# Performance work log

Hardware: AMD Instinct MI355X
Metric: run time of the kernel (lower is better)

## Reference

```python
import jax, jax.numpy as jnp
import numpy as np

NUM_HEADS = 8
IN_CH = 256  # C per branch; x has 2*C channels
DHW = (16, 16, 16)


def _proj(w, b, feat):
    # 1x1x1 Conv3d == per-voxel linear over channels. w: [Co, Ci], feat: [B, Ci, D, H, W]
    return jnp.einsum('oc,bcdhw->bodhw', w, feat) + b[None, :, None, None, None]


def _rope(n, dim):
    # matches rotary_embedding: returns [dim, n]
    inv_freq = 1.0 / (10000.0 ** (jnp.arange(0, dim, 2, dtype=jnp.float32) / dim))
    pos = jnp.linspace(-1.0, 1.0, n)
    sinusoid = pos[:, None] * inv_freq[None, :]          # [n, dim//2]
    emb = jnp.concatenate([jnp.sin(sinusoid), jnp.cos(sinusoid)], axis=-1)  # [n, dim]
    return emb.T                                          # [dim, n]


def setup_inputs() -> dict:
    key = jax.random.key(0)
    ks = jax.random.split(key, 5)
    D, H, W = DHW
    C = IN_CH
    s = 0.05
    return {
        'x': jax.random.normal(ks[0], (1, 2 * C, D, H, W), dtype=jnp.float32),
        'wq': jax.random.normal(ks[1], (C, C), dtype=jnp.float32) * s,
        'bq': jnp.zeros((C,), jnp.float32),
        'wk': jax.random.normal(ks[2], (C, C), dtype=jnp.float32) * s,
        'bk': jnp.zeros((C,), jnp.float32),
        'wv': jax.random.normal(ks[3], (C, C), dtype=jnp.float32) * s,
        'bv': jnp.zeros((C,), jnp.float32),
        'wo': jax.random.normal(ks[4], (2 * C, C), dtype=jnp.float32) * s,
        'bo': jnp.zeros((2 * C,), jnp.float32),
    }


def reference(x, wq, bq, wk, bk, wv, bv, wo, bo):
    qf, kvf = jnp.split(x, 2, axis=1)          # each [B, C, D, H, W]
    B, C, D, H, W = qf.shape
    hd = C // NUM_HEADS
    N = D * H * W
    q = _proj(wq, bq, qf).reshape(B, NUM_HEADS, hd, N)
    k = _proj(wk, bk, kvf).reshape(B, NUM_HEADS, hd, N)
    v = _proj(wv, bv, kvf).reshape(B, NUM_HEADS, hd, N)
    pe = _rope(N, hd)                           # [hd, N]
    q = q * pe[None, None]
    k = k * pe[None, None]
    attn = jnp.einsum('bhcn,bhcm->bhnm', q, k)  # note: no 1/sqrt(d) scaling, as in source
    attn = jax.nn.softmax(attn, axis=-1)
    out = jnp.einsum('bhnm,bhcm->bhcn', attn, v).reshape(B, C, D, H, W)
    return _proj(wo, bo, out + qf)              # [B, 2C, D, H, W]
```

## Files before the change

kernel.cpp:

```cpp
#include <hip/hip_runtime.h>
#include <hip/hip_bf16.h>

#define CIN 256
#define NV 4096
#define NHEAD 8
#define HD 32
#define NSPLIT 2
#define KSPAN (NV / NSPLIT)
#define LOG2E 1.44269504088896340736f
#define LOG2_10K_16 0.8304820237218405f

typedef __attribute__((ext_vector_type(8))) short short8;
typedef __attribute__((ext_vector_type(4))) float f32x4;

static __device__ __forceinline__ unsigned short f2bf(float f) {
    union { float f; unsigned u; } v; v.f = f;
    unsigned r = v.u + 0x7fffu + ((v.u >> 16) & 1u);
    return (unsigned short)(r >> 16);
}
static __device__ __forceinline__ unsigned pk_bf2(float x0, float x1) {
    return __builtin_amdgcn_perm(__float_as_uint(x1), __float_as_uint(x0),
                                 0x07060302u);
}
static __device__ __forceinline__ float bflo(unsigned u) {
    return __uint_as_float(u << 16);
}
static __device__ __forceinline__ float bfhi(unsigned u) {
    return __uint_as_float(u & 0xffff0000u);
}

__global__ __launch_bounds__(256) void conv_w(
    const float* __restrict__ wq, const float* __restrict__ wk,
    const float* __restrict__ wv, const float* __restrict__ wo,
    unsigned short* __restrict__ Wb)
{
    int i = (blockIdx.x * 256 + threadIdx.x) * 4;
    if (i >= 327680) return;
    const float* src;
    int off = i;
    if (i < 65536) { src = wq; }
    else if (i < 131072) { src = wk; off = i - 65536; }
    else if (i < 196608) { src = wv; off = i - 131072; }
    else { src = wo; off = i - 196608; }
    float4 v = *(const float4*)&src[off];
    unsigned short pk[4] = {f2bf(v.x), f2bf(v.y), f2bf(v.z), f2bf(v.w)};
    *(uint2*)&Wb[i] = *(uint2*)pk;
}

__global__ __launch_bounds__(512) void qkv_fused(
    const float* __restrict__ x, const unsigned short* __restrict__ Wb,
    const float* __restrict__ bq, const float* __restrict__ bk,
    const float* __restrict__ bv,
    unsigned short* __restrict__ Qbf, unsigned short* __restrict__ Kbf,
    unsigned short* __restrict__ Vbf)
{
    const int which = blockIdx.z;
    const unsigned short* Wp = Wb + (size_t)which * 65536;
    const float* Bp = (which == 0) ? bq : (which == 1) ? bk : bv;
    const int cbase = (which == 0) ? 0 : CIN;

    const int n0 = blockIdx.x * 64;
    const int m0 = blockIdx.y * 128;
    const int t = threadIdx.x;

    __shared__ __align__(16) unsigned short Sbuf[128 * 136];

    {
        const int n = t & 63, cg = t >> 6;
#pragma unroll 4
        for (int cc = 0; cc < 32; cc += 2) {
            const int c = cg * 32 + cc;
            size_t off = (size_t)(cbase + c) * NV + n0 + n;
            *(unsigned*)&Sbuf[n * 264 + c] = pk_bf2(x[off], x[off + NV]);
        }
    }
    __syncthreads();

    const int w = t >> 6;
    const int lane = t & 63;
    const int ln = lane & 15;
    const int quad = lane >> 4;
    const int M = m0 + w * 16 + ln;

    f32x4 acc[4] = {};
    const unsigned short* Wrow = &Wp[(size_t)M * 256 + quad * 8];
    for (int k0 = 0; k0 < 256; k0 += 32) {
        short8 a = *(const short8*)&Wrow[k0];
        short8 b[4];
#pragma unroll
        for (int nt = 0; nt < 4; ++nt)
            b[nt] = *(const short8*)&Sbuf[(nt * 16 + ln) * 264 + k0 + quad * 8];
        if (which == 2) {
#pragma unroll
            for (int nt = 0; nt < 4; ++nt)
                acc[nt] = __builtin_amdgcn_mfma_f32_16x16x32_bf16(
                    b[nt], a, acc[nt], 0, 0, 0);
        } else {
#pragma unroll
            for (int nt = 0; nt < 4; ++nt)
                acc[nt] = __builtin_amdgcn_mfma_f32_16x16x32_bf16(
                    a, b[nt], acc[nt], 0, 0, 0);
        }
    }
    __syncthreads();

    if (which == 2) {
        const int cl = w * 16 + ln;
        const float bias = Bp[m0 + cl];
#pragma unroll
        for (int nt = 0; nt < 4; ++nt) {
            unsigned short pk4[4];
#pragma unroll
            for (int r = 0; r < 4; ++r) pk4[r] = f2bf(acc[nt][r] + bias);
            *(uint2*)&Sbuf[cl * 136 + nt * 16 + quad * 4] = *(uint2*)pk4;
        }
        __syncthreads();
#pragma unroll
        for (int j = 0; j < 2; ++j) {
            int gid = j * 512 + t;
            int n8 = (gid & 7) * 8, cl2 = gid >> 3;
            uint4 v = *(const uint4*)&Sbuf[cl2 * 136 + n8];
            *(uint4*)&Vbf[(size_t)(m0 + cl2) * NV + n0 + n8] = v;
        }
    } else {
        const int mb = m0 + w * 16 + quad * 4;
        const int cb = mb & 31;
        const float qscale = (which == 0) ? LOG2E : 1.0f;
        float bias[4], invf[4];
#pragma unroll
        for (int r = 0; r < 4; ++r) {
            bias[r] = Bp[mb + r];
            invf[r] = __builtin_amdgcn_exp2f(
                -(float)((cb + r) & 15) * LOG2_10K_16);
        }
        const bool use_sin = (cb < 16);
        const int ml = w * 16 + quad * 4;
#pragma unroll
        for (int nt = 0; nt < 4; ++nt) {
            const int n = n0 + nt * 16 + ln;
            const float pos = (float)n * (2.0f / 4095.0f) - 1.0f;
#pragma unroll
            for (int r = 0; r < 4; ++r) {
                float ang = pos * invf[r];
                float f = (use_sin ? __sinf(ang) : __cosf(ang)) * qscale;
                Sbuf[(nt * 16 + ln) * 264 + ml + r] =
                    f2bf((acc[nt][r] + bias[r]) * f);
            }
        }
        __syncthreads();
        unsigned short* dst = (which == 0) ? Qbf : Kbf;
        const int h0 = m0 >> 5;
#pragma unroll
        for (int j = 0; j < 2; ++j) {
            int gid = j * 512 + t;
            int c8 = (gid & 3) * 8;
            int n = (gid >> 2) & 63;
            int hh = gid >> 8;
            uint4 v = *(const uint4*)&Sbuf[n * 264 + hh * 32 + c8];
            *(uint4*)&dst[((size_t)(h0 + hh) * NV + n0 + n) * HD + c8] = v;
        }
    }
}

__global__ __launch_bounds__(256, 4) void attn_mfma(
    const unsigned short* __restrict__ Qbf,
    const unsigned short* __restrict__ Kbf,
    const unsigned short* __restrict__ Vbf,
    unsigned short* __restrict__ Opartb, float* __restrict__ Lpart)
{
    const int h = blockIdx.y;
    const int q0 = blockIdx.x * 64;
    const int z = blockIdx.z;
    const int kbase = z * KSPAN;
    const int t = threadIdx.x;
    const int w = t >> 6;
    const int lane = t & 63;
    const int ln = lane & 15;
    const int quad = lane >> 4;

    __shared__ __align__(16) unsigned short Vs[2][2048];

    const short8 qa = *(const short8*)
        &Qbf[((size_t)h * NV + q0 + w * 16 + ln) * HD + quad * 8];

    const unsigned short* Kh = Kbf + (size_t)h * NV * HD;
    const unsigned short* Vh = Vbf + (size_t)h * HD * NV;

    const int c_st = (w << 3) + (lane >> 3);
    const int gr_st = (lane & 7) ^ (c_st & 7);
    const unsigned short* gsrc = Vh + (size_t)c_st * NV + gr_st * 8;
    unsigned short* lds0 = &Vs[0][(size_t)(w * 64 + lane) * 8];
    unsigned short* lds1 = &Vs[1][(size_t)(w * 64 + lane) * 8];

    f32x4 oacc[2] = {};
    f32x4 lacc = {};
    const short vone = (short)0x3F80;
    const short8 vones = {vone, vone, vone, vone, vone, vone, vone, vone};

    __builtin_amdgcn_global_load_lds(
        (const __attribute__((address_space(1))) unsigned int*)(gsrc + kbase),
        (__attribute__((address_space(3))) unsigned int*)lds0, 16, 0, 0);
    short8 kf[4];
#pragma unroll
    for (int ct = 0; ct < 4; ++ct)
        kf[ct] = *(const short8*)
            &Kh[(size_t)(kbase + ct * 16 + ln) * HD + quad * 8];
    __syncthreads();

    for (int i = 0; i < KSPAN / 64; ++i) {
        const int kb = kbase + i * 64;
        const int buf = i & 1;

        if (i + 1 < KSPAN / 64) {
            __builtin_amdgcn_global_load_lds(
                (const __attribute__((address_space(1))) unsigned int*)(gsrc + kb + 64),
                (__attribute__((address_space(3))) unsigned int*)(buf ? lds0 : lds1),
                16, 0, 0);
        }
        const int kbn = kbase + (((i + 1) & (KSPAN / 64 - 1)) * 64);
        short8 kfn[4];
#pragma unroll
        for (int ct = 0; ct < 4; ++ct)
            kfn[ct] = *(const short8*)
                &Kh[(size_t)(kbn + ct * 16 + ln) * HD + quad * 8];

        f32x4 s[4];
#pragma unroll
        for (int ct = 0; ct < 4; ++ct) {
            f32x4 z4 = {0.f, 0.f, 0.f, 0.f};
            s[ct] = __builtin_amdgcn_mfma_f32_16x16x32_bf16(kf[ct], qa, z4,
                                                            0, 0, 0);
        }

        float p[4][4];
#pragma unroll
        for (int ct = 0; ct < 4; ++ct)
#pragma unroll
            for (int r = 0; r < 4; ++r)
                p[ct][r] = __builtin_amdgcn_exp2f(s[ct][r]);

#pragma unroll
        for (int h2 = 0; h2 < 2; ++h2) {
            short8 pa;
            unsigned* pau = (unsigned*)&pa;
            pau[0] = pk_bf2(p[2 * h2][0], p[2 * h2][1]);
            pau[1] = pk_bf2(p[2 * h2][2], p[2 * h2][3]);
            pau[2] = pk_bf2(p[2 * h2 + 1][0], p[2 * h2 + 1][1]);
            pau[3] = pk_bf2(p[2 * h2 + 1][2], p[2 * h2 + 1][3]);
            lacc = __builtin_amdgcn_mfma_f32_16x16x32_bf16(pa, vones, lacc,
                                                           0, 0, 0);
#pragma unroll
            for (int ctile = 0; ctile < 2; ++ctile) {
                const int cA = ctile * 16 + ln;
                short8 vb;
                unsigned* vbu = (unsigned*)&vb;
#pragma unroll
                for (int g = 0; g < 2; ++g) {
                    const int gr = h2 * 4 + g * 2 + (quad >> 1);
                    const int sg = gr ^ (ln & 7);
                    uint2 vv = *(const uint2*)
                        &Vs[buf][cA * 64 + sg * 8 + (quad & 1) * 4];
                    vbu[g * 2 + 0] = vv.x;
                    vbu[g * 2 + 1] = vv.y;
                }
                oacc[ctile] = __builtin_amdgcn_mfma_f32_16x16x32_bf16(
                    pa, vb, oacc[ctile], 0, 0, 0);
            }
        }

#pragma unroll
        for (int ct = 0; ct < 4; ++ct) kf[ct] = kfn[ct];
        __syncthreads();
    }

    unsigned short* Oz = Opartb + (size_t)z * CIN * NV;
    float* Lz = Lpart + (size_t)z * NHEAD * NV;
    if (ln == 0) {
#pragma unroll
        for (int r = 0; r < 4; ++r)
            Lz[(size_t)h * NV + q0 + w * 16 + quad * 4 + r] = lacc[r];
    }
#pragma unroll
    for (int ctile = 0; ctile < 2; ++ctile) {
        uint2 st;
        st.x = pk_bf2(oacc[ctile][0], oacc[ctile][1]);
        st.y = pk_bf2(oacc[ctile][2], oacc[ctile][3]);
        *(uint2*)&Oz[(size_t)(h * HD + ctile * 16 + ln) * NV + q0 + w * 16 +
                     quad * 4] = st;
    }
}

__global__ __launch_bounds__(512) void out_fused(
    const float* __restrict__ x,
    const unsigned short* __restrict__ O0b,
    const unsigned short* __restrict__ O1b,
    const float* __restrict__ Lpart,
    const unsigned short* __restrict__ Wob, const float* __restrict__ bo,
    float* __restrict__ out)
{
    const int n0 = blockIdx.x * 64;
    const int m0 = blockIdx.y * 128;
    const int t = threadIdx.x;

    __shared__ __align__(16) unsigned short Ys[64 * 264];

    const float* L0 = Lpart;
    const float* L1 = Lpart + (size_t)NHEAD * NV;

    {
        const int n2 = (t & 31) * 2;
        const int grp = t >> 5;
        const int h = grp >> 1;
        const size_t lo = (size_t)h * NV + n0 + n2;
        const float rl0 = __builtin_amdgcn_rcpf(L0[lo] + L1[lo]);
        const float rl1 = __builtin_amdgcn_rcpf(L0[lo + 1] + L1[lo + 1]);
#pragma unroll 4
        for (int i = 0; i < 16; ++i) {
            const int c = grp * 16 + i;
            size_t off = (size_t)c * NV + n0 + n2;
            unsigned o0 = *(const unsigned*)&O0b[off];
            unsigned o1 = *(const unsigned*)&O1b[off];
            float2 x2 = *(const float2*)&x[off];
            float y0 = (bflo(o0) + bflo(o1)) * rl0 + x2.x;
            float y1 = (bfhi(o0) + bfhi(o1)) * rl1 + x2.y;
            Ys[n2 * 264 + c] = f2bf(y0);
            Ys[(n2 + 1) * 264 + c] = f2bf(y1);
        }
    }
    __syncthreads();

    const int w = t >> 6;
    const int lane = t & 63;
    const int ln = lane & 15;
    const int quad = lane >> 4;
    const int M = m0 + w * 16 + ln;

    const unsigned short* Wrow = &Wob[(size_t)M * 256 + quad * 8];
    f32x4 acc[4] = {};
    for (int k0 = 0; k0 < 256; k0 += 32) {
        short8 a = *(const short8*)&Wrow[k0];
        short8 b[4];
#pragma unroll
        for (int nt = 0; nt < 4; ++nt)
            b[nt] = *(const short8*)&Ys[(nt * 16 + ln) * 264 + k0 + quad * 8];
#pragma unroll
        for (int nt = 0; nt < 4; ++nt)
            acc[nt] = __builtin_amdgcn_mfma_f32_16x16x32_bf16(
                a, b[nt], acc[nt], 0, 0, 0);
    }

    const int mb = m0 + w * 16 + quad * 4;
    float bias[4];
#pragma unroll
    for (int r = 0; r < 4; ++r) bias[r] = bo[mb + r];
#pragma unroll
    for (int nt = 0; nt < 4; ++nt)
#pragma unroll
        for (int r = 0; r < 4; ++r)
            out[(size_t)(mb + r) * NV + n0 + nt * 16 + ln] =
                acc[nt][r] + bias[r];
}

extern "C" void kernel_launch(void* const* d_in, const int* in_sizes, int n_in,
                              void* d_out, int out_size, void* d_ws,
                              size_t ws_size, hipStream_t stream)
{
    const float* x  = (const float*)d_in[0];
    const float* wq = (const float*)d_in[1];
    const float* bq = (const float*)d_in[2];
    const float* wk = (const float*)d_in[3];
    const float* bk = (const float*)d_in[4];
    const float* wv = (const float*)d_in[5];
    const float* bv = (const float*)d_in[6];
    const float* wo = (const float*)d_in[7];
    const float* bo = (const float*)d_in[8];
    float* out = (float*)d_out;

    unsigned short* Wb  = (unsigned short*)d_ws;
    unsigned short* Qbf = Wb + 327680;
    unsigned short* Kbf = Qbf + (size_t)CIN * NV;
    unsigned short* Vbf = Kbf + (size_t)CIN * NV;
    float* Lpart = (float*)(Vbf + (size_t)CIN * NV);
    unsigned short* Opartb =
        (unsigned short*)(Lpart + 2 * (size_t)NHEAD * NV);

    conv_w<<<dim3(320), 256, 0, stream>>>(wq, wk, wv, wo, Wb);
    qkv_fused<<<dim3(64, 2, 3), 512, 0, stream>>>(
        x, Wb, bq, bk, bv, Qbf, Kbf, Vbf);
    attn_mfma<<<dim3(NV / 64, NHEAD, NSPLIT), 256, 0, stream>>>(
        Qbf, Kbf, Vbf, Opartb, Lpart);
    out_fused<<<dim3(64, 4), 512, 0, stream>>>(
        x, Opartb, Opartb + (size_t)CIN * NV, Lpart, Wb + 196608, bo, out);
}
```

Measured before the change: 129.0 us.

## Split attention keys four ways, stage K in LDS, shrink projection tiles

Raises the key-split factor for attention from 2 to 4, so twice as many blocks run and the GPU is filled more evenly. The partial outputs and normalisers are reduced generically in the output kernel. K tiles now go into swizzled LDS through async global_load_lds, double-buffered alongside V, replacing per-lane register prefetch. The V fragment read becomes a single 16-byte LDS load. The QKV and output projection kernels halve their voxel tile to 32 to double the grid. The costs are more partial-sum traffic and reduction work in the epilogue, and less reuse per projection block.

```diff
diff --git a/kernel.cpp b/kernel.cpp
--- a/kernel.cpp
+++ b/kernel.cpp
@@ -5,7 +5,7 @@
 #define NV 4096
 #define NHEAD 8
 #define HD 32
-#define NSPLIT 2
+#define NSPLIT 4
 #define KSPAN (NV / NSPLIT)
 #define LOG2E 1.44269504088896340736f
 #define LOG2_10K_16 0.8304820237218405f
@@ -59,17 +59,17 @@
     const float* Bp = (which == 0) ? bq : (which == 1) ? bk : bv;
     const int cbase = (which == 0) ? 0 : CIN;
 
-    const int n0 = blockIdx.x * 64;
+    const int n0 = blockIdx.x * 32;
     const int m0 = blockIdx.y * 128;
     const int t = threadIdx.x;
 
-    __shared__ __align__(16) unsigned short Sbuf[128 * 136];
+    __shared__ __align__(16) unsigned short Sbuf[32 * 264];
 
     {
-        const int n = t & 63, cg = t >> 6;
+        const int n = t & 31, cg = t >> 5;
 #pragma unroll 4
-        for (int cc = 0; cc < 32; cc += 2) {
-            const int c = cg * 32 + cc;
+        for (int cc = 0; cc < 16; cc += 2) {
+            const int c = cg * 16 + cc;
             size_t off = (size_t)(cbase + c) * NV + n0 + n;
             *(unsigned*)&Sbuf[n * 264 + c] = pk_bf2(x[off], x[off + NV]);
         }
@@ -82,22 +82,22 @@
     const int quad = lane >> 4;
     const int M = m0 + w * 16 + ln;
 
-    f32x4 acc[4] = {};
+    f32x4 acc[2] = {};
     const unsigned short* Wrow = &Wp[(size_t)M * 256 + quad * 8];
     for (int k0 = 0; k0 < 256; k0 += 32) {
         short8 a = *(const short8*)&Wrow[k0];
-        short8 b[4];
-#pragma unroll
-        for (int nt = 0; nt < 4; ++nt)
+        short8 b[2];
+#pragma unroll
+        for (int nt = 0; nt < 2; ++nt)
             b[nt] = *(const short8*)&Sbuf[(nt * 16 + ln) * 264 + k0 + quad * 8];
         if (which == 2) {
 #pragma unroll
-            for (int nt = 0; nt < 4; ++nt)
+            for (int nt = 0; nt < 2; ++nt)
                 acc[nt] = __builtin_amdgcn_mfma_f32_16x16x32_bf16(
                     b[nt], a, acc[nt], 0, 0, 0);
         } else {
 #pragma unroll
-            for (int nt = 0; nt < 4; ++nt)
+            for (int nt = 0; nt < 2; ++nt)
                 acc[nt] = __builtin_amdgcn_mfma_f32_16x16x32_bf16(
                     a, b[nt], acc[nt], 0, 0, 0);
         }
@@ -108,19 +108,20 @@
         const int cl = w * 16 + ln;
         const float bias = Bp[m0 + cl];
 #pragma unroll
-        for (int nt = 0; nt < 4; ++nt) {
+        for (int nt = 0; nt < 2; ++nt) {
             unsigned short pk4[4];
 #pragma unroll
             for (int r = 0; r < 4; ++r) pk4[r] = f2bf(acc[nt][r] + bias);
-            *(uint2*)&Sbuf[cl * 136 + nt * 16 + quad * 4] = *(uint2*)pk4;
+            *(uint2*)&Sbuf[cl * 40 + nt * 16 + quad * 4] = *(uint2*)pk4;
         }
         __syncthreads();
-#pragma unroll
-        for (int j = 0; j < 2; ++j) {
-            int gid = j * 512 + t;
-            int n8 = (gid & 7) * 8, cl2 = gid >> 3;
-            uint4 v = *(const uint4*)&Sbuf[cl2 * 136 + n8];
-            *(uint4*)&Vbf[(size_t)(m0 + cl2) * NV + n0 + n8] = v;
+        {
+            const int cl2 = t >> 2, q = t & 3;
+            uint2 lo = *(const uint2*)&Sbuf[cl2 * 40 + q * 4];
+            uint2 hi = *(const uint2*)&Sbuf[cl2 * 40 + 16 + q * 4];
+            uint4 v;
+            v.x = lo.x; v.y = lo.y; v.z = hi.x; v.w = hi.y;
+            *(uint4*)&Vbf[(size_t)(m0 + cl2) * NV + n0 + q * 8] = v;
         }
     } else {
         const int mb = m0 + w * 16 + quad * 4;
@@ -136,7 +137,7 @@
         const bool use_sin = (cb < 16);
         const int ml = w * 16 + quad * 4;
 #pragma unroll
-        for (int nt = 0; nt < 4; ++nt) {
+        for (int nt = 0; nt < 2; ++nt) {
             const int n = n0 + nt * 16 + ln;
             const float pos = (float)n * (2.0f / 4095.0f) - 1.0f;
 #pragma unroll
@@ -150,14 +151,12 @@
         __syncthreads();
         unsigned short* dst = (which == 0) ? Qbf : Kbf;
         const int h0 = m0 >> 5;
-#pragma unroll
-        for (int j = 0; j < 2; ++j) {
-            int gid = j * 512 + t;
-            int c8 = (gid & 3) * 8;
-            int n = (gid >> 2) & 63;
-            int hh = gid >> 8;
-            uint4 v = *(const uint4*)&Sbuf[n * 264 + hh * 32 + c8];
-            *(uint4*)&dst[((size_t)(h0 + hh) * NV + n0 + n) * HD + c8] = v;
+        {
+            const int hh = t >> 7;
+            const int n = (t >> 2) & 31;
+            const int cw = t & 3;
+            uint4 v = *(const uint4*)&Sbuf[n * 264 + hh * 32 + cw * 8];
+            *(uint4*)&dst[((size_t)(h0 + hh) * NV + n0 + n) * HD + cw * 8] = v;
         }
     }
 }
@@ -178,6 +177,7 @@
     const int ln = lane & 15;
     const int quad = lane >> 4;
 
+    __shared__ __align__(16) unsigned short Ks[2][2048];
     __shared__ __align__(16) unsigned short Vs[2][2048];
 
     const short8 qa = *(const short8*)
@@ -186,11 +186,11 @@
     const unsigned short* Kh = Kbf + (size_t)h * NV * HD;
     const unsigned short* Vh = Vbf + (size_t)h * HD * NV;
 
-    const int c_st = (w << 3) + (lane >> 3);
-    const int gr_st = (lane & 7) ^ (c_st & 7);
-    const unsigned short* gsrc = Vh + (size_t)c_st * NV + gr_st * 8;
-    unsigned short* lds0 = &Vs[0][(size_t)(w * 64 + lane) * 8];
-    unsigned short* lds1 = &Vs[1][(size_t)(w * 64 + lane) * 8];
+    const int cv = t >> 3;
+    const unsigned short* gsrcV = Vh + (size_t)cv * NV + ((t & 7) ^ (cv & 7)) * 8;
+    const int kv = t >> 2;
+    const unsigned short* gsrcK =
+        Kh + (size_t)kv * HD + ((t & 3) ^ (kv & 3)) * 8;
 
     f32x4 oacc[2] = {};
     f32x4 lacc = {};
@@ -198,37 +198,39 @@
     const short8 vones = {vone, vone, vone, vone, vone, vone, vone, vone};
 
     __builtin_amdgcn_global_load_lds(
-        (const __attribute__((address_space(1))) unsigned int*)(gsrc + kbase),
-        (__attribute__((address_space(3))) unsigned int*)lds0, 16, 0, 0);
-    short8 kf[4];
-#pragma unroll
-    for (int ct = 0; ct < 4; ++ct)
-        kf[ct] = *(const short8*)
-            &Kh[(size_t)(kbase + ct * 16 + ln) * HD + quad * 8];
+        (const __attribute__((address_space(1))) unsigned int*)(gsrcK +
+            (size_t)kbase * HD),
+        (__attribute__((address_space(3))) unsigned int*)&Ks[0][t * 8], 16, 0, 0);
+    __builtin_amdgcn_global_load_lds(
+        (const __attribute__((address_space(1))) unsigned int*)(gsrcV + kbase),
+        (__attribute__((address_space(3))) unsigned int*)&Vs[0][t * 8], 16, 0, 0);
     __syncthreads();
 
+    const int sgk = (quad ^ (ln & 3)) * 8;
     for (int i = 0; i < KSPAN / 64; ++i) {
         const int kb = kbase + i * 64;
         const int buf = i & 1;
 
         if (i + 1 < KSPAN / 64) {
             __builtin_amdgcn_global_load_lds(
-                (const __attribute__((address_space(1))) unsigned int*)(gsrc + kb + 64),
-                (__attribute__((address_space(3))) unsigned int*)(buf ? lds0 : lds1),
+                (const __attribute__((address_space(1))) unsigned int*)(gsrcK +
+                    (size_t)(kb + 64) * HD),
+                (__attribute__((address_space(3))) unsigned int*)&Ks[buf ^ 1][t * 8],
                 16, 0, 0);
-        }
-        const int kbn = kbase + (((i + 1) & (KSPAN / 64 - 1)) * 64);
-        short8 kfn[4];
-#pragma unroll
-        for (int ct = 0; ct < 4; ++ct)
-            kfn[ct] = *(const short8*)
-                &Kh[(size_t)(kbn + ct * 16 + ln) * HD + quad * 8];
+            __builtin_amdgcn_global_load_lds(
+                (const __attribute__((address_space(1))) unsigned int*)(gsrcV +
+                    kb + 64),
+                (__attribute__((address_space(3))) unsigned int*)&Vs[buf ^ 1][t * 8],
+                16, 0, 0);
+        }
 
         f32x4 s[4];
 #pragma unroll
         for (int ct = 0; ct < 4; ++ct) {
+            const short8 kf = *(const short8*)
+                &Ks[buf][(ct * 16 + ln) * 32 + sgk];
             f32x4 z4 = {0.f, 0.f, 0.f, 0.f};
-            s[ct] = __builtin_amdgcn_mfma_f32_16x16x32_bf16(kf[ct], qa, z4,
+            s[ct] = __builtin_amdgcn_mfma_f32_16x16x32_bf16(kf, qa, z4,
                                                             0, 0, 0);
         }
 
@@ -252,24 +254,12 @@
 #pragma unroll
             for (int ctile = 0; ctile < 2; ++ctile) {
                 const int cA = ctile * 16 + ln;
-                short8 vb;
-                unsigned* vbu = (unsigned*)&vb;
-#pragma unroll
-                for (int g = 0; g < 2; ++g) {
-                    const int gr = h2 * 4 + g * 2 + (quad >> 1);
-                    const int sg = gr ^ (ln & 7);
-                    uint2 vv = *(const uint2*)
-                        &Vs[buf][cA * 64 + sg * 8 + (quad & 1) * 4];
-                    vbu[g * 2 + 0] = vv.x;
-                    vbu[g * 2 + 1] = vv.y;
-                }
+                const short8 vb = *(const short8*)
+                    &Vs[buf][cA * 64 + (((h2 * 4 + quad) ^ (cA & 7)) * 8)];
                 oacc[ctile] = __builtin_amdgcn_mfma_f32_16x16x32_bf16(
                     pa, vb, oacc[ctile], 0, 0, 0);
             }
         }
-
-#pragma unroll
-        for (int ct = 0; ct < 4; ++ct) kf[ct] = kfn[ct];
         __syncthreads();
     }
 
@@ -292,39 +282,44 @@
 
 __global__ __launch_bounds__(512) void out_fused(
     const float* __restrict__ x,
-    const unsigned short* __restrict__ O0b,
-    const unsigned short* __restrict__ O1b,
+    const unsigned short* __restrict__ Opartb,
     const float* __restrict__ Lpart,
     const unsigned short* __restrict__ Wob, const float* __restrict__ bo,
     float* __restrict__ out)
 {
-    const int n0 = blockIdx.x * 64;
+    const int n0 = blockIdx.x * 32;
     const int m0 = blockIdx.y * 128;
     const int t = threadIdx.x;
 
-    __shared__ __align__(16) unsigned short Ys[64 * 264];
-
-    const float* L0 = Lpart;
-    const float* L1 = Lpart + (size_t)NHEAD * NV;
+    __shared__ __align__(16) unsigned short Ys[32 * 264];
 
     {
-        const int n2 = (t & 31) * 2;
-        const int grp = t >> 5;
-        const int h = grp >> 1;
+        const int n2 = (t & 15) * 2;
+        const int grp = t >> 4;
+        const int h = grp >> 2;
         const size_t lo = (size_t)h * NV + n0 + n2;
-        const float rl0 = __builtin_amdgcn_rcpf(L0[lo] + L1[lo]);
-        const float rl1 = __builtin_amdgcn_rcpf(L0[lo + 1] + L1[lo + 1]);
-#pragma unroll 4
-        for (int i = 0; i < 16; ++i) {
-            const int c = grp * 16 + i;
+        float l0 = 0.f, l1 = 0.f;
+#pragma unroll
+        for (int zz = 0; zz < NSPLIT; ++zz) {
+            l0 += Lpart[(size_t)zz * NHEAD * NV + lo];
+            l1 += Lpart[(size_t)zz * NHEAD * NV + lo + 1];
+        }
+        const float rl0 = __builtin_amdgcn_rcpf(l0);
+        const float rl1 = __builtin_amdgcn_rcpf(l1);
+#pragma unroll
+        for (int i = 0; i < 8; ++i) {
+            const int c = grp * 8 + i;
             size_t off = (size_t)c * NV + n0 + n2;
-            unsigned o0 = *(const unsigned*)&O0b[off];
-            unsigned o1 = *(const unsigned*)&O1b[off];
+            float s0 = 0.f, s1 = 0.f;
+#pragma unroll
+            for (int zz = 0; zz < NSPLIT; ++zz) {
+                unsigned o = *(const unsigned*)&Opartb[(size_t)zz * CIN * NV + off];
+                s0 += bflo(o);
+                s1 += bfhi(o);
+            }
             float2 x2 = *(const float2*)&x[off];
-            float y0 = (bflo(o0) + bflo(o1)) * rl0 + x2.x;
-            float y1 = (bfhi(o0) + bfhi(o1)) * rl1 + x2.y;
-            Ys[n2 * 264 + c] = f2bf(y0);
-            Ys[(n2 + 1) * 264 + c] = f2bf(y1);
+            Ys[n2 * 264 + c] = f2bf(s0 * rl0 + x2.x);
+            Ys[(n2 + 1) * 264 + c] = f2bf(s1 * rl1 + x2.y);
         }
     }
     __syncthreads();
@@ -336,15 +331,15 @@
     const int M = m0 + w * 16 + ln;
 
     const unsigned short* Wrow = &Wob[(size_t)M * 256 + quad * 8];
-    f32x4 acc[4] = {};
+    f32x4 acc[2] = {};
     for (int k0 = 0; k0 < 256; k0 += 32) {
         short8 a = *(const short8*)&Wrow[k0];
-        short8 b[4];
-#pragma unroll
-        for (int nt = 0; nt < 4; ++nt)
+        short8 b[2];
+#pragma unroll
+        for (int nt = 0; nt < 2; ++nt)
             b[nt] = *(const short8*)&Ys[(nt * 16 + ln) * 264 + k0 + quad * 8];
 #pragma unroll
-        for (int nt = 0; nt < 4; ++nt)
+        for (int nt = 0; nt < 2; ++nt)
             acc[nt] = __builtin_amdgcn_mfma_f32_16x16x32_bf16(
                 a, b[nt], acc[nt], 0, 0, 0);
     }
@@ -354,7 +349,7 @@
 #pragma unroll
     for (int r = 0; r < 4; ++r) bias[r] = bo[mb + r];
 #pragma unroll
-    for (int nt = 0; nt < 4; ++nt)
+    for (int nt = 0; nt < 2; ++nt)
 #pragma unroll
         for (int r = 0; r < 4; ++r)
             out[(size_t)(mb + r) * NV + n0 + nt * 16 + ln] =
@@ -382,13 +377,13 @@
     unsigned short* Vbf = Kbf + (size_t)CIN * NV;
     float* Lpart = (float*)(Vbf + (size_t)CIN * NV);
     unsigned short* Opartb =
-        (unsigned short*)(Lpart + 2 * (size_t)NHEAD * NV);
+        (unsigned short*)(Lpart + NSPLIT * (size_t)NHEAD * NV);
 
     conv_w<<<dim3(320), 256, 0, stream>>>(wq, wk, wv, wo, Wb);
-    qkv_fused<<<dim3(64, 2, 3), 512, 0, stream>>>(
+    qkv_fused<<<dim3(128, 2, 3), 512, 0, stream>>>(
         x, Wb, bq, bk, bv, Qbf, Kbf, Vbf);
     attn_mfma<<<dim3(NV / 64, NHEAD, NSPLIT), 256, 0, stream>>>(
         Qbf, Kbf, Vbf, Opartb, Lpart);
-    out_fused<<<dim3(64, 4), 512, 0, stream>>>(
-        x, Opartb, Opartb + (size_t)CIN * NV, Lpart, Wb + 196608, bo, out);
-}
+    out_fused<<<dim3(128, 4), 512, 0, stream>>>(
+        x, Opartb, Lpart, Wb + 196608, bo, out);
+}
```

Result: faster. 120.5 us (-6.6%).
